# Kernel optimization log

Hardware: AMD Instinct MI355X
Metric: run time of the kernel (lower is better)

## Reference

```python
import jax, jax.numpy as jnp
import numpy as np

# NF4 codebook (bitsandbytes / torchao canonical 16 levels)
_NF4 = np.array([
    -1.0, -0.6961928009986877, -0.5250730514526367, -0.39491748809814453,
    -0.28444138169288635, -0.18477343022823334, -0.09105003625154495, 0.0,
    0.07958029955625534, 0.16093020141124725, 0.24611230194568634,
    0.33791524171829224, 0.44070982933044434, 0.5626170039176941,
    0.7229568362236023, 1.0], dtype=np.float32)

IN_DIM = 4096
OUT_DIM = 4096
RANK = 16
ALPHA = 32.0
BLOCK = 64  # NF4 quantization block size along in_dim


def setup_inputs() -> dict:
    key = jax.random.key(0)
    k1, k2, k3, k4, k5 = jax.random.split(key, 5)
    x = jax.random.normal(k1, (4, 2048, IN_DIM), dtype=jnp.float32)
    # 4-bit codes for the frozen base weight [out_dim, in_dim]
    w_q = jax.random.randint(k2, (OUT_DIM, IN_DIM), 0, 16, dtype=jnp.int32)
    # per-block absmax scales: [out_dim, in_dim // BLOCK]
    scales = jax.random.uniform(k3, (OUT_DIM, IN_DIM // BLOCK), dtype=jnp.float32)
    lora_a_w = jax.random.normal(k4, (RANK, IN_DIM), dtype=jnp.float32) * (1.0 / np.sqrt(IN_DIM))
    lora_b_w = jax.random.normal(k5, (OUT_DIM, RANK), dtype=jnp.float32) * 0.02
    return {"x": x, "w_q": w_q, "scales": scales,
            "lora_a_w": lora_a_w, "lora_b_w": lora_b_w}


def _dequant_nf4(w_q, scales):
    # w_q: [out, in] int codes; scales: [out, in//BLOCK]
    codebook = jnp.asarray(_NF4)
    w = codebook[w_q]  # [out, in]
    w = w.reshape(w.shape[0], -1, BLOCK) * scales[:, :, None]
    return w.reshape(w_q.shape)  # [out, in]


def reference(x, w_q, scales, lora_a_w, lora_b_w):
    # base path: dequantized NF4 linear (frozen, no bias)
    w = _dequant_nf4(w_q, scales)          # [out, in]
    out = jnp.einsum('bsi,oi->bso', x, w)  # [B, S, out]
    # LoRA path: dropout is Identity (p=0.0)
    a = jnp.einsum('bsi,ri->bsr', x, lora_a_w)      # [B, S, r]
    lora_out = jnp.einsum('bsr,or->bso', a, lora_b_w)  # [B, S, out]
    return out + (ALPHA / RANK) * lora_out
```

## Files before the change

### kernel.cpp

```cpp
#include <hip/hip_runtime.h>

typedef unsigned int u32;
typedef unsigned short u16;
typedef __bf16 bf16x8 __attribute__((ext_vector_type(8)));
typedef float f32x4 __attribute__((ext_vector_type(4)));

#define M_TOT 8192
#define N_TOT 4096
#define K_TOT 4096
#define RANK 16

#define BM 256
#define BN 256
#define BK 64
#define NT (K_TOT / BK)

#define CVT_BLOCKS 16384

__constant__ float NF4_TAB[16] = {
    -1.0f, -0.6961928009986877f, -0.5250730514526367f, -0.39491748809814453f,
    -0.28444138169288635f, -0.18477343022823334f, -0.09105003625154495f, 0.0f,
    0.07958029955625534f, 0.16093020141124725f, 0.24611230194568634f,
    0.33791524171829224f, 0.44070982933044434f, 0.5626170039176941f,
    0.7229568362236023f, 1.0f};

__device__ __forceinline__ u16 f2bf(float f) {
  u32 u = __builtin_bit_cast(u32, f);
  return (u16)((u + 0x7FFFu + ((u >> 16) & 1u)) >> 16);
}

__device__ __forceinline__ void async_copy16(const u16* g, u16* l) {
  __builtin_amdgcn_global_load_lds(
      (const __attribute__((address_space(1))) u32*)g,
      (__attribute__((address_space(3))) u32*)l, 16, 0, 0);
}

__global__ __launch_bounds__(256) void prep_kernel(
    const float* __restrict__ x, u16* __restrict__ xb,
    const int* __restrict__ wq, const float* __restrict__ scales,
    const float* __restrict__ Aw, const float* __restrict__ Bw,
    u16* __restrict__ Wb) {
  if (blockIdx.x < CVT_BLOCKS) {
    int t = blockIdx.x * 256 + threadIdx.x;
    const float4* xv = (const float4*)x;
    float4 v0 = xv[2 * t], v1 = xv[2 * t + 1];
    uint4 o;
    o.x = (u32)f2bf(v0.x) | ((u32)f2bf(v0.y) << 16);
    o.y = (u32)f2bf(v0.z) | ((u32)f2bf(v0.w) << 16);
    o.z = (u32)f2bf(v1.x) | ((u32)f2bf(v1.y) << 16);
    o.w = (u32)f2bf(v1.z) | ((u32)f2bf(v1.w) << 16);
    ((uint4*)xb)[t] = o;
    return;
  }
  int db = blockIdx.x - CVT_BLOCKS;
  int bx = db & 3, by = db >> 2;

  __shared__ float Bs[16 * RANK];
  int t = threadIdx.x;
  int o0 = by * 16;
  int tabi = __builtin_bit_cast(int, NF4_TAB[t & 15]);
  Bs[t] = Bw[o0 * RANK + t];
  __syncthreads();

  int i0 = bx * 1024 + t * 4;
  float a[RANK][4];
#pragma unroll
  for (int r = 0; r < RANK; ++r) {
    float4 v = *(const float4*)(Aw + r * K_TOT + i0);
    a[r][0] = v.x; a[r][1] = v.y; a[r][2] = v.z; a[r][3] = v.w;
  }
#pragma unroll
  for (int j = 0; j < 16; ++j) {
    int o = o0 + j;
    int4 q = *(const int4*)(wq + (size_t)o * K_TOT + i0);
    float s = scales[o * (K_TOT / 64) + (i0 >> 6)];
    float d0 = 0.f, d1 = 0.f, d2 = 0.f, d3 = 0.f;
#pragma unroll
    for (int r = 0; r < RANK; ++r) {
      float b = Bs[j * RANK + r];
      d0 += b * a[r][0]; d1 += b * a[r][1];
      d2 += b * a[r][2]; d3 += b * a[r][3];
    }
    float t0 = __builtin_bit_cast(float, __builtin_amdgcn_ds_bpermute((q.x & 15) << 2, tabi));
    float t1 = __builtin_bit_cast(float, __builtin_amdgcn_ds_bpermute((q.y & 15) << 2, tabi));
    float t2 = __builtin_bit_cast(float, __builtin_amdgcn_ds_bpermute((q.z & 15) << 2, tabi));
    float t3 = __builtin_bit_cast(float, __builtin_amdgcn_ds_bpermute((q.w & 15) << 2, tabi));
    float w0 = t0 * s + 2.0f * d0;
    float w1 = t1 * s + 2.0f * d1;
    float w2 = t2 * s + 2.0f * d2;
    float w3 = t3 * s + 2.0f * d3;
    uint2 ov;
    ov.x = (u32)f2bf(w0) | ((u32)f2bf(w1) << 16);
    ov.y = (u32)f2bf(w2) | ((u32)f2bf(w3) << 16);
    *(uint2*)(Wb + (size_t)o * K_TOT + i0) = ov;
  }
}

#define STAGE_A(buf, k0, i) \
  async_copy16(gA + (size_t)(i) * 64 * K_TOT + (k0), &sh[buf][0][(i) * 4096 + tid * 8])
#define STAGE_B(buf, k0, i) \
  async_copy16(gB + (size_t)(i) * 64 * K_TOT + (k0), &sh[buf][1][(i) * 4096 + tid * 8])

#define LOAD_A(mh)                                              \
  do {                                                          \
    const u16* p_ = sA + (wm * 128 + (mh) * 64 + m) * 64;       \
    _Pragma("unroll") for (int i_ = 0; i_ < 4; ++i_) {          \
      af[i_][0] = *(const bf16x8*)(p_ + i_ * 16 * 64 + off0);   \
      af[i_][1] = *(const bf16x8*)(p_ + i_ * 16 * 64 + off1);   \
    }                                                           \
  } while (0)

#define LOAD_B(nh)                                                        \
  do {                                                                    \
    const u16* p_ = sB + (wn * 64 + (nh) * 32 + m) * 64;                  \
    _Pragma("unroll") for (int j_ = 0; j_ < 2; ++j_) {                    \
      bfr[(nh) * 2 + j_][0] = *(const bf16x8*)(p_ + j_ * 16 * 64 + off0); \
      bfr[(nh) * 2 + j_][1] = *(const bf16x8*)(p_ + j_ * 16 * 64 + off1); \
    }                                                                     \
  } while (0)

#define PHASE_TAIL(mh, nh)                                                  \
  do {                                                                      \
    __builtin_amdgcn_s_barrier();                                           \
    asm volatile("s_waitcnt lgkmcnt(0)" ::: "memory");                      \
    __builtin_amdgcn_sched_barrier(0);                                      \
    __builtin_amdgcn_s_setprio(1);                                          \
    _Pragma("unroll") for (int kk_ = 0; kk_ < 2; ++kk_)                     \
    _Pragma("unroll") for (int i_ = 0; i_ < 4; ++i_)                        \
    _Pragma("unroll") for (int j_ = 0; j_ < 2; ++j_)                        \
      acc[(mh) * 4 + i_][(nh) * 2 + j_] =                                   \
          __builtin_amdgcn_mfma_f32_16x16x32_bf16(                          \
              af[i_][kk_], bfr[(nh) * 2 + j_][kk_],                         \
              acc[(mh) * 4 + i_][(nh) * 2 + j_], 0, 0, 0);                  \
    __builtin_amdgcn_s_setprio(0);                                          \
    __builtin_amdgcn_s_barrier();                                           \
  } while (0)

__global__ __launch_bounds__(512, 2) void gemm_kernel(const u16* __restrict__ A,
                                                      const u16* __restrict__ B,
                                                      float* __restrict__ C) {
  __shared__ __align__(16) u16 sh[2][2][BM * BK];

  int tid = threadIdx.x;
  int lane = tid & 63, wave = tid >> 6;
  int wm = wave >> 2, wn = wave & 3;

  int bid = blockIdx.y * gridDim.x + blockIdx.x;
  int swz = (bid & 7) * 64 + (bid >> 3);
  int bm = swz >> 4, bn = swz & 15;

  int srow = tid >> 3;
  int sg = (tid & 7) ^ (srow & 7);
  const u16* gA = A + (size_t)(bm * BM + srow) * K_TOT + sg * 8;
  const u16* gB = B + (size_t)(bn * BN + srow) * K_TOT + sg * 8;

  int m = lane & 15, q = lane >> 4;
  int x7 = m & 7;
  int off0 = (q ^ x7) << 3;
  int off1 = ((q + 4) ^ x7) << 3;

  f32x4 acc[8][4] = {};
  bf16x8 af[4][2], bfr[4][2];

#pragma unroll
  for (int i = 0; i < 4; ++i) {
    STAGE_A(0, 0, i);
    STAGE_B(0, 0, i);
  }

  for (int t = 0; t < NT - 1; ++t) {
    int cur = t & 1, nxt = cur ^ 1;
    int k1 = (t + 1) * BK;
    const u16* sA = sh[cur][0];
    const u16* sB = sh[cur][1];

#pragma unroll
    for (int i = 0; i < 4; ++i) STAGE_A(nxt, k1, i);
    asm volatile("s_waitcnt vmcnt(4)" ::: "memory");
    __builtin_amdgcn_s_barrier();

    LOAD_A(0);
    LOAD_B(0);
    STAGE_B(nxt, k1, 0);
    STAGE_B(nxt, k1, 1);
    asm volatile("s_waitcnt lgkmcnt(8)" ::: "memory");
    PHASE_TAIL(0, 0);

    LOAD_B(1);
    STAGE_B(nxt, k1, 2);
    STAGE_B(nxt, k1, 3);
    PHASE_TAIL(0, 1);

    LOAD_A(1);
    PHASE_TAIL(1, 1);

    PHASE_TAIL(1, 0);
  }

  {
    const u16* sA = sh[(NT - 1) & 1][0];
    const u16* sB = sh[(NT - 1) & 1][1];
    asm volatile("s_waitcnt vmcnt(0)" ::: "memory");
    __builtin_amdgcn_s_barrier();
    LOAD_A(0);
    LOAD_B(0);
    asm volatile("s_waitcnt lgkmcnt(8)" ::: "memory");
    PHASE_TAIL(0, 0);
    LOAD_B(1);
    PHASE_TAIL(0, 1);
    LOAD_A(1);
    PHASE_TAIL(1, 1);
    PHASE_TAIL(1, 0);
  }

  int r0 = bm * BM + wm * 128 + (q << 2);
  int c0 = bn * BN + wn * 64 + m;
#pragma unroll
  for (int i = 0; i < 8; ++i)
#pragma unroll
    for (int j = 0; j < 4; ++j)
#pragma unroll
      for (int p = 0; p < 4; ++p)
        C[(size_t)(r0 + i * 16 + p) * N_TOT + (c0 + j * 16)] = acc[i][j][p];
}

extern "C" void kernel_launch(void* const* d_in, const int* in_sizes, int n_in,
                              void* d_out, int out_size, void* d_ws, size_t ws_size,
                              hipStream_t stream) {
  const float* x = (const float*)d_in[0];
  const int* wq = (const int*)d_in[1];
  const float* scales = (const float*)d_in[2];
  const float* Aw = (const float*)d_in[3];
  const float* Bw = (const float*)d_in[4];
  float* out = (float*)d_out;

  u16* xb = (u16*)d_ws;
  u16* Wb = (u16*)((char*)d_ws + (size_t)M_TOT * K_TOT * 2);

  prep_kernel<<<CVT_BLOCKS + (K_TOT / 1024) * (N_TOT / 16), 256, 0, stream>>>(
      x, xb, wq, scales, Aw, Bw, Wb);
  gemm_kernel<<<dim3(N_TOT / BN, M_TOT / BM), 512, 0, stream>>>(xb, Wb, out);
}
```

Measured before the change: 514.2 us.

## Software-pipeline GEMM staging across half-tiles and reorder prep block dispatch

The GEMM main loop is unrolled by two, and the global-to-LDS async copies for the next tile are spread across the four MFMA phases. Some of them target the buffer just consumed within the same iteration, so the separate vmcnt wait plus barrier at the head of each k-step is gone and copy latency overlaps with compute. The prep kernel now puts the heavier dequant blocks first in the grid so they start early and do not form a tail. The tighter interleaving relies on the vmcnt counts and barrier placement being exactly right to avoid LDS races.

```diff
diff --git a/kernel.cpp b/kernel.cpp
--- a/kernel.cpp
+++ b/kernel.cpp
@@ -15,6 +15,7 @@
 #define BK 64
 #define NT (K_TOT / BK)
 
+#define DQ_BLOCKS 1024
 #define CVT_BLOCKS 16384
 
 __constant__ float NF4_TAB[16] = {
@@ -40,8 +41,8 @@
     const int* __restrict__ wq, const float* __restrict__ scales,
     const float* __restrict__ Aw, const float* __restrict__ Bw,
     u16* __restrict__ Wb) {
-  if (blockIdx.x < CVT_BLOCKS) {
-    int t = blockIdx.x * 256 + threadIdx.x;
+  if (blockIdx.x >= DQ_BLOCKS) {
+    int t = (blockIdx.x - DQ_BLOCKS) * 256 + threadIdx.x;
     const float4* xv = (const float4*)x;
     float4 v0 = xv[2 * t], v1 = xv[2 * t + 1];
     uint4 o;
@@ -52,8 +53,7 @@
     ((uint4*)xb)[t] = o;
     return;
   }
-  int db = blockIdx.x - CVT_BLOCKS;
-  int bx = db & 3, by = db >> 2;
+  int bx = blockIdx.x & 3, by = blockIdx.x >> 2;
 
   __shared__ float Bs[16 * RANK];
   int t = threadIdx.x;
@@ -119,21 +119,34 @@
     }                                                                     \
   } while (0)
 
-#define PHASE_TAIL(mh, nh)                                                  \
-  do {                                                                      \
-    __builtin_amdgcn_s_barrier();                                           \
-    asm volatile("s_waitcnt lgkmcnt(0)" ::: "memory");                      \
-    __builtin_amdgcn_sched_barrier(0);                                      \
-    __builtin_amdgcn_s_setprio(1);                                          \
-    _Pragma("unroll") for (int kk_ = 0; kk_ < 2; ++kk_)                     \
-    _Pragma("unroll") for (int i_ = 0; i_ < 4; ++i_)                        \
-    _Pragma("unroll") for (int j_ = 0; j_ < 2; ++j_)                        \
-      acc[(mh) * 4 + i_][(nh) * 2 + j_] =                                   \
-          __builtin_amdgcn_mfma_f32_16x16x32_bf16(                          \
-              af[i_][kk_], bfr[(nh) * 2 + j_][kk_],                         \
-              acc[(mh) * 4 + i_][(nh) * 2 + j_], 0, 0, 0);                  \
-    __builtin_amdgcn_s_setprio(0);                                          \
-    __builtin_amdgcn_s_barrier();                                           \
+#define MFMA_QUAD(mh, nh)                                                   \
+  _Pragma("unroll") for (int kk_ = 0; kk_ < 2; ++kk_)                       \
+  _Pragma("unroll") for (int i_ = 0; i_ < 4; ++i_)                          \
+  _Pragma("unroll") for (int j_ = 0; j_ < 2; ++j_)                          \
+    acc[(mh) * 4 + i_][(nh) * 2 + j_] =                                     \
+        __builtin_amdgcn_mfma_f32_16x16x32_bf16(                            \
+            af[i_][kk_], bfr[(nh) * 2 + j_][kk_],                           \
+            acc[(mh) * 4 + i_][(nh) * 2 + j_], 0, 0, 0)
+
+#define PHASE_TAIL(mh, nh)                                 \
+  do {                                                     \
+    __builtin_amdgcn_s_barrier();                          \
+    asm volatile("s_waitcnt lgkmcnt(0)" ::: "memory");     \
+    __builtin_amdgcn_s_setprio(1);                         \
+    MFMA_QUAD(mh, nh);                                     \
+    __builtin_amdgcn_s_setprio(0);                         \
+    __builtin_amdgcn_s_barrier();                          \
+  } while (0)
+
+#define PHASE_TAIL_VM(mh, nh, vmstr)                       \
+  do {                                                     \
+    __builtin_amdgcn_s_barrier();                          \
+    asm volatile("s_waitcnt lgkmcnt(0)" ::: "memory");     \
+    __builtin_amdgcn_s_setprio(1);                         \
+    MFMA_QUAD(mh, nh);                                     \
+    __builtin_amdgcn_s_setprio(0);                         \
+    asm volatile("s_waitcnt " vmstr ::: "memory");         \
+    __builtin_amdgcn_s_barrier();                          \
   } while (0)
 
 __global__ __launch_bounds__(512, 2) void gemm_kernel(const u16* __restrict__ A,
@@ -163,45 +176,82 @@
   bf16x8 af[4][2], bfr[4][2];
 
 #pragma unroll
-  for (int i = 0; i < 4; ++i) {
-    STAGE_A(0, 0, i);
-    STAGE_B(0, 0, i);
-  }
-
-  for (int t = 0; t < NT - 1; ++t) {
-    int cur = t & 1, nxt = cur ^ 1;
-    int k1 = (t + 1) * BK;
-    const u16* sA = sh[cur][0];
-    const u16* sB = sh[cur][1];
-
-#pragma unroll
-    for (int i = 0; i < 4; ++i) STAGE_A(nxt, k1, i);
-    asm volatile("s_waitcnt vmcnt(4)" ::: "memory");
-    __builtin_amdgcn_s_barrier();
-
+  for (int i = 0; i < 4; ++i) STAGE_A(0, 0, i);
+#pragma unroll
+  for (int i = 0; i < 4; ++i) STAGE_B(0, 0, i);
+  STAGE_A(1, BK, 0);
+  STAGE_A(1, BK, 2);
+#pragma unroll
+  for (int i = 0; i < 4; ++i) STAGE_B(1, BK, i);
+  asm volatile("s_waitcnt vmcnt(6)" ::: "memory");
+  __builtin_amdgcn_s_barrier();
+
+  for (int J = 0; J < NT / 2 - 1; ++J) {
+    int k1 = (2 * J + 1) * BK;
+    int k2 = k1 + BK;
+    int k3 = k2 + BK;
+    {
+      const u16* sA = sh[0][0];
+      const u16* sB = sh[0][1];
+      LOAD_A(0);
+      LOAD_B(0);
+      STAGE_A(1, k1, 1);
+      STAGE_A(1, k1, 3);
+      asm volatile("s_waitcnt lgkmcnt(8)" ::: "memory");
+      PHASE_TAIL(0, 0);
+      LOAD_B(1);
+      STAGE_A(0, k2, 0);
+      STAGE_A(0, k2, 2);
+      PHASE_TAIL(0, 1);
+      LOAD_A(1);
+      STAGE_B(0, k2, 0);
+      STAGE_B(0, k2, 1);
+      PHASE_TAIL(1, 1);
+      STAGE_B(0, k2, 2);
+      STAGE_B(0, k2, 3);
+      PHASE_TAIL_VM(1, 0, "vmcnt(6)");
+    }
+    {
+      const u16* sA = sh[1][0];
+      const u16* sB = sh[1][1];
+      LOAD_A(0);
+      LOAD_B(0);
+      STAGE_A(0, k2, 1);
+      STAGE_A(0, k2, 3);
+      asm volatile("s_waitcnt lgkmcnt(8)" ::: "memory");
+      PHASE_TAIL(0, 0);
+      LOAD_B(1);
+      STAGE_A(1, k3, 0);
+      STAGE_A(1, k3, 2);
+      PHASE_TAIL(0, 1);
+      LOAD_A(1);
+      STAGE_B(1, k3, 0);
+      STAGE_B(1, k3, 1);
+      PHASE_TAIL(1, 1);
+      STAGE_B(1, k3, 2);
+      STAGE_B(1, k3, 3);
+      PHASE_TAIL_VM(1, 0, "vmcnt(6)");
+    }
+  }
+
+  {
+    const u16* sA = sh[0][0];
+    const u16* sB = sh[0][1];
     LOAD_A(0);
     LOAD_B(0);
-    STAGE_B(nxt, k1, 0);
-    STAGE_B(nxt, k1, 1);
+    STAGE_A(1, (NT - 1) * BK, 1);
+    STAGE_A(1, (NT - 1) * BK, 3);
     asm volatile("s_waitcnt lgkmcnt(8)" ::: "memory");
     PHASE_TAIL(0, 0);
-
     LOAD_B(1);
-    STAGE_B(nxt, k1, 2);
-    STAGE_B(nxt, k1, 3);
     PHASE_TAIL(0, 1);
-
     LOAD_A(1);
     PHASE_TAIL(1, 1);
-
-    PHASE_TAIL(1, 0);
-  }
-
+    PHASE_TAIL_VM(1, 0, "vmcnt(0)");
+  }
   {
-    const u16* sA = sh[(NT - 1) & 1][0];
-    const u16* sB = sh[(NT - 1) & 1][1];
-    asm volatile("s_waitcnt vmcnt(0)" ::: "memory");
-    __builtin_amdgcn_s_barrier();
+    const u16* sA = sh[1][0];
+    const u16* sB = sh[1][1];
     LOAD_A(0);
     LOAD_B(0);
     asm volatile("s_waitcnt lgkmcnt(8)" ::: "memory");
@@ -237,7 +287,7 @@
   u16* xb = (u16*)d_ws;
   u16* Wb = (u16*)((char*)d_ws + (size_t)M_TOT * K_TOT * 2);
 
-  prep_kernel<<<CVT_BLOCKS + (K_TOT / 1024) * (N_TOT / 16), 256, 0, stream>>>(
+  prep_kernel<<<DQ_BLOCKS + CVT_BLOCKS, 256, 0, stream>>>(
       x, xb, wq, scales, Aw, Bw, Wb);
   gemm_kernel<<<dim3(N_TOT / BN, M_TOT / BM), 512, 0, stream>>>(xb, Wb, out);
 }
```

Result: faster. 483.9 us (-5.9%).
